# Performance work log

Hardware: AMD Instinct MI355X
Metric: run time of the kernel (lower is better)

The kernel has to match this reference:

```python
import jax, jax.numpy as jnp
import numpy as np

NHEADS = 16
LORA_SCALE = 16.0 / 16.0  # alpha / r


def lora_linear(x, W, b, A, B):
    # base projection + low-rank LoRA path: x@W^T + b + s*(x@A^T)@B^T
    base = jnp.einsum('bse,oe->bso', x, W) + b
    low = jnp.einsum('bse,re->bsr', x, A)  # [B,S,r]
    return base + LORA_SCALE * jnp.einsum('bsr,or->bso', low, B)


def setup_inputs() -> dict:
    key = jax.random.key(0)
    E, R = 1024, 16
    ks = jax.random.split(key, 20)
    d = {'x': jax.random.normal(ks[0], (4, 1024, E), jnp.float32)}
    i = 1
    for p in ('q', 'k', 'v', 'o'):
        d[f'{p}_w'] = jax.random.normal(ks[i], (E, E), jnp.float32) * 0.02; i += 1
        d[f'{p}_b'] = jax.random.normal(ks[i], (E,), jnp.float32) * 0.02; i += 1
        d[f'{p}_la'] = jax.random.normal(ks[i], (R, E), jnp.float32) * 0.02; i += 1
        d[f'{p}_lb'] = jax.random.normal(ks[i], (E, R), jnp.float32) * 0.02; i += 1
    return d


def reference(x, q_w, q_b, q_la, q_lb, k_w, k_b, k_la, k_lb,
              v_w, v_b, v_la, v_lb, o_w, o_b, o_la, o_lb):
    B, S, E = x.shape
    H = NHEADS
    D = E // H
    q = lora_linear(x, q_w, q_b, q_la, q_lb).reshape(B, S, H, D)
    k = lora_linear(x, k_w, k_b, k_la, k_lb).reshape(B, S, H, D)
    v = lora_linear(x, v_w, v_b, v_la, v_lb).reshape(B, S, H, D)
    scores = jnp.einsum('bshd,bthd->bhst', q, k) / jnp.sqrt(jnp.asarray(D, x.dtype))
    attn = jax.nn.softmax(scores, axis=-1)
    ctx = jnp.einsum('bhst,bthd->bshd', attn, v).reshape(B, S, E)
    return lora_linear(ctx, o_w, o_b, o_la, o_lb)
```

## Files before the change

### kernel.cpp

```cpp
#include <hip/hip_runtime.h>
#include <cstdint>


typedef __attribute__((ext_vector_type(8))) short bf16x8;
typedef __attribute__((ext_vector_type(4))) float f32x4;
typedef __attribute__((ext_vector_type(16))) float f32x16;
typedef __attribute__((ext_vector_type(4))) unsigned short u16x4;
typedef __attribute__((ext_vector_type(4))) unsigned int u32x4;

__device__ __forceinline__ short f2bf(float f) {
  unsigned u = __builtin_bit_cast(unsigned, f);
  u += 0x7FFFu + ((u >> 16) & 1u);
  return (short)(u >> 16);
}

typedef __attribute__((address_space(1))) const unsigned int as1_uint;
typedef __attribute__((address_space(3))) unsigned int as3_uint;

__device__ __forceinline__ void gload_lds16(const short* g, const short* l) {
  __builtin_amdgcn_global_load_lds((as1_uint*)g,
      (as3_uint*)(unsigned int)(uintptr_t)l, 16, 0, 0);
}

__device__ __forceinline__ unsigned cvtpk(float lo, float hi) {
  unsigned r;
  asm("v_cvt_pk_bf16_f32 %0, %1, %2" : "=v"(r) : "v"(lo), "v"(hi));
  return r;
}
__device__ __forceinline__ void plswap(unsigned &a, unsigned &b) {
  asm("v_permlane32_swap_b32 %0, %1" : "+v"(a), "+v"(b));
}

__device__ __forceinline__ void build_pfrag(const f32x16 &s, bf16x8 &f0, bf16x8 &f1) {
  unsigned x0 = cvtpk(s[0], s[1]),  x1 = cvtpk(s[2], s[3]);
  unsigned x2 = cvtpk(s[4], s[5]),  x3 = cvtpk(s[6], s[7]);
  plswap(x0, x2); plswap(x1, x3);
  unsigned y0 = cvtpk(s[8], s[9]),  y1 = cvtpk(s[10], s[11]);
  unsigned y2 = cvtpk(s[12], s[13]), y3 = cvtpk(s[14], s[15]);
  plswap(y0, y2); plswap(y1, y3);
  u32x4 a = {x0, x1, x2, x3}, b = {y0, y1, y2, y3};
  f0 = __builtin_bit_cast(bf16x8, a);
  f1 = __builtin_bit_cast(bf16x8, b);
}

__global__ void build_x(const float* __restrict__ x, short* __restrict__ xb) {
  int idx = blockIdx.x * 256 + threadIdx.x;
  f32x4 v = ((const f32x4*)x)[idx];
  u16x4 o;
  o[0] = (unsigned short)f2bf(v[0]);
  o[1] = (unsigned short)f2bf(v[1]);
  o[2] = (unsigned short)f2bf(v[2]);
  o[3] = (unsigned short)f2bf(v[3]);
  ((u16x4*)xb)[idx] = o;
}

__global__ void fold_w(const float* __restrict__ wq, const float* __restrict__ wk,
                       const float* __restrict__ wv, const float* __restrict__ wo,
                       const float* __restrict__ bq, const float* __restrict__ bk,
                       const float* __restrict__ bv, const float* __restrict__ bo,
                       const float* __restrict__ aq, const float* __restrict__ ak,
                       const float* __restrict__ av, const float* __restrict__ ao,
                       short* __restrict__ out) {
  const int p = blockIdx.y;
  const float* W  = (p == 0) ? wq : (p == 1) ? wk : (p == 2) ? wv : wo;
  const float* Bm = (p == 0) ? bq : (p == 1) ? bk : (p == 2) ? bv : bo;
  const float* A  = (p == 0) ? aq : (p == 1) ? ak : (p == 2) ? av : ao;
  const int idx = blockIdx.x * 256 + threadIdx.x;
  const int n = idx >> 8;
  const int e4 = idx & 255;
  f32x4 acc = ((const f32x4*)(W + (size_t)n * 1024))[e4];
  const float* br = Bm + n * 16;
  #pragma unroll
  for (int r = 0; r < 16; ++r) {
    const f32x4 a4 = ((const f32x4*)(A + (size_t)r * 1024))[e4];
    const float b = br[r];
    acc[0] += b * a4[0];
    acc[1] += b * a4[1];
    acc[2] += b * a4[2];
    acc[3] += b * a4[3];
  }
  u16x4 o;
  o[0] = (unsigned short)f2bf(acc[0]);
  o[1] = (unsigned short)f2bf(acc[1]);
  o[2] = (unsigned short)f2bf(acc[2]);
  o[3] = (unsigned short)f2bf(acc[3]);
  *(u16x4*)(out + (size_t)p * 1048576 + (size_t)idx * 4) = o;
}

__device__ __forceinline__ void gemm_core(const short* __restrict__ xrow,
                                          const short* __restrict__ wrow,
                                          short* As, short* Bs,
                                          f32x4 (&acc)[4][4]) {
  const int tid = threadIdx.x;
  const int wv = tid >> 6, lane = tid & 63;
  const int wr = wv >> 1, wc = wv & 1;
  const int lrow = lane & 15, lk = lane >> 4;
  const int srow = lane >> 3, sphys = lane & 7;

  for (int kt = 0; kt < 16; ++kt) {
    #pragma unroll
    for (int i = 0; i < 4; ++i) {
      const int ch = i * 4 + wv;
      const int row = ch * 8 + srow;
      const int sl = sphys ^ (row & 7);
      gload_lds16(xrow + (size_t)row * 1024 + kt * 64 + sl * 8, As + ch * 512);
      gload_lds16(wrow + (size_t)row * 1024 + kt * 64 + sl * 8, Bs + ch * 512);
    }
    __syncthreads();
    #pragma unroll
    for (int kc = 0; kc < 2; ++kc) {
      bf16x8 af[4], bw[4];
      #pragma unroll
      for (int mi = 0; mi < 4; ++mi) {
        const int row = wr * 64 + mi * 16 + lrow;
        const int slot = (kc * 4 + lk) ^ (row & 7);
        af[mi] = *(const bf16x8*)(As + row * 64 + slot * 8);
      }
      #pragma unroll
      for (int nj = 0; nj < 4; ++nj) {
        const int row = wc * 64 + nj * 16 + lrow;
        const int slot = (kc * 4 + lk) ^ (row & 7);
        bw[nj] = *(const bf16x8*)(Bs + row * 64 + slot * 8);
      }
      #pragma unroll
      for (int mi = 0; mi < 4; ++mi)
        #pragma unroll
        for (int nj = 0; nj < 4; ++nj)
          acc[mi][nj] = __builtin_amdgcn_mfma_f32_16x16x32_bf16(af[mi], bw[nj], acc[mi][nj], 0, 0, 0);
    }
    __syncthreads();
  }
}

__global__ __launch_bounds__(256)
void gemm_qkv(const short* __restrict__ xb, const short* __restrict__ wb,
              const float* __restrict__ biasq, const float* __restrict__ biask,
              const float* __restrict__ biasv,
              short* __restrict__ qbuf, short* __restrict__ kbuf, short* __restrict__ vtb) {
  __shared__ short As[128 * 64];
  __shared__ short Bs[128 * 64];
  const int p = blockIdx.z;
  const int brow = blockIdx.y, bcol = blockIdx.x;
  const f32x4 fz = {0.f, 0.f, 0.f, 0.f};
  f32x4 acc[4][4];
  #pragma unroll
  for (int a = 0; a < 4; ++a)
    #pragma unroll
    for (int b = 0; b < 4; ++b) acc[a][b] = fz;

  gemm_core(xb + (size_t)brow * 128 * 1024,
            wb + ((size_t)p * 1024 + (size_t)bcol * 128) * 1024, As, Bs, acc);

  const int tid = threadIdx.x;
  const int wv = tid >> 6, lane = tid & 63;
  const int wr = wv >> 1, wc = wv & 1;
  const int lrow = lane & 15, lk = lane >> 4;
  const float* bias = (p == 0) ? biasq : (p == 1) ? biask : biasv;
  const float oscale = (p == 0) ? 0.18033688f : 1.0f;
  float bcv[4];
  #pragma unroll
  for (int nj = 0; nj < 4; ++nj)
    bcv[nj] = bias[bcol * 128 + wc * 64 + nj * 16 + lrow];

  #pragma unroll
  for (int mi = 0; mi < 4; ++mi) {
    #pragma unroll
    for (int r = 0; r < 4; ++r) {
      const int gr = brow * 128 + wr * 64 + mi * 16 + lk * 4 + r;
      const int bb = gr >> 10, s = gr & 1023;
      #pragma unroll
      for (int nj = 0; nj < 4; ++nj) {
        const int gc = bcol * 128 + wc * 64 + nj * 16 + lrow;
        const float v = (acc[mi][nj][r] + bcv[nj]) * oscale;
        const int h = gc >> 6, d = gc & 63;
        const int bh = bb * 16 + h;
        if (p == 2)
          vtb[((size_t)bh * 64 + d) * 1024 + s] = f2bf(v);
        else
          ((p == 0) ? qbuf : kbuf)[((size_t)bh * 1024 + s) * 64 + d] = f2bf(v);
      }
    }
  }
}

__global__ __launch_bounds__(256)
void attn_kernel(const short* __restrict__ qbuf, const short* __restrict__ kbuf,
                 const short* __restrict__ vtb, short* __restrict__ cb) {
  __shared__ short Ks[2][64 * 64];
  __shared__ short Vs[2][64 * 64];
  const int bh = blockIdx.x, qt = blockIdx.y;
  const int tid = threadIdx.x, w = tid >> 6, lane = tid & 63;
  const int l31 = lane & 31, hi = lane >> 5;
  const int srow = lane >> 3, sphys = lane & 7;
  const short* Qp = qbuf + (size_t)bh * 65536;
  const short* Kp = kbuf + (size_t)bh * 65536;
  const short* Vp = vtb + (size_t)bh * 65536;
  const int q0 = qt * 128 + w * 32;

  bf16x8 bq[4];
  #pragma unroll
  for (int kc = 0; kc < 4; ++kc)
    bq[kc] = *(const bf16x8*)(Qp + (size_t)(q0 + l31) * 64 + kc * 16 + hi * 8);

  const f32x16 fz16 = {0.f,0.f,0.f,0.f,0.f,0.f,0.f,0.f,0.f,0.f,0.f,0.f,0.f,0.f,0.f,0.f};
  float m_run = -1e30f, l_run = 0.f;
  f32x16 acc0 = fz16, acc1 = fz16;

  #define STAGE_KV(buf, tt)                                                  \
    {                                                                        \
      const int t0s = (tt) * 64;                                             \
      _Pragma("unroll")                                                      \
      for (int i = 0; i < 2; ++i) {                                          \
        const int ch = i * 4 + w;                                            \
        const int row = ch * 8 + srow;                                       \
        const int sl = sphys ^ (row & 7);                                    \
        gload_lds16(Kp + (size_t)(t0s + row) * 64 + sl * 8, Ks[buf] + ch * 512); \
        gload_lds16(Vp + (size_t)row * 1024 + t0s + sl * 8, Vs[buf] + ch * 512); \
      }                                                                      \
    }

  STAGE_KV(0, 0);
  __syncthreads();

  int cur = 0;
  for (int tt = 0; tt < 16; ++tt) {
    if (tt < 15) STAGE_KV(cur ^ 1, tt + 1);

    f32x16 s0 = fz16, s1 = fz16;
    #pragma unroll
    for (int kc = 0; kc < 4; ++kc) {
      const int slot = (kc * 2 + hi) ^ (l31 & 7);
      const bf16x8 ak0 = *(const bf16x8*)(Ks[cur] + l31 * 64 + slot * 8);
      const bf16x8 ak1 = *(const bf16x8*)(Ks[cur] + (32 + l31) * 64 + slot * 8);
      s0 = __builtin_amdgcn_mfma_f32_32x32x16_bf16(ak0, bq[kc], s0, 0, 0, 0);
      s1 = __builtin_amdgcn_mfma_f32_32x32x16_bf16(ak1, bq[kc], s1, 0, 0, 0);
    }

    float tm = s0[0];
    #pragma unroll
    for (int r = 1; r < 16; ++r) tm = fmaxf(tm, s0[r]);
    #pragma unroll
    for (int r = 0; r < 16; ++r) tm = fmaxf(tm, s1[r]);
    tm = fmaxf(tm, __shfl_xor(tm, 32, 64));
    const float mn = fmaxf(m_run, tm);
    const float alpha = exp2f(m_run - mn);
    m_run = mn;
    float rs = 0.f;
    #pragma unroll
    for (int r = 0; r < 16; ++r) { const float p = exp2f(s0[r] - mn); s0[r] = p; rs += p; }
    #pragma unroll
    for (int r = 0; r < 16; ++r) { const float p = exp2f(s1[r] - mn); s1[r] = p; rs += p; }
    rs += __shfl_xor(rs, 32, 64);
    l_run = l_run * alpha + rs;
    #pragma unroll
    for (int r = 0; r < 16; ++r) { acc0[r] *= alpha; acc1[r] *= alpha; }

    bf16x8 pf[4];
    build_pfrag(s0, pf[0], pf[1]);
    build_pfrag(s1, pf[2], pf[3]);

    #pragma unroll
    for (int kc4 = 0; kc4 < 4; ++kc4) {
      const int slot = (kc4 * 2 + hi) ^ (l31 & 7);
      const bf16x8 av0 = *(const bf16x8*)(Vs[cur] + l31 * 64 + slot * 8);
      const bf16x8 av1 = *(const bf16x8*)(Vs[cur] + (32 + l31) * 64 + slot * 8);
      acc0 = __builtin_amdgcn_mfma_f32_32x32x16_bf16(av0, pf[kc4], acc0, 0, 0, 0);
      acc1 = __builtin_amdgcn_mfma_f32_32x32x16_bf16(av1, pf[kc4], acc1, 0, 0, 0);
    }

    __syncthreads();
    cur ^= 1;
  }

  const int bb = bh >> 4, h = bh & 15;
  const int s = q0 + l31;
  short* crow = cb + (size_t)(bb * 1024 + s) * 1024 + h * 64;
  const float inv = 1.f / l_run;
  #pragma unroll
  for (int rp = 0; rp < 8; ++rp) {
    const int r = rp * 2;
    const int d = (r & 3) + 8 * (r >> 2) + 4 * hi;
    const unsigned p0 = (unsigned)(unsigned short)f2bf(acc0[r] * inv)
                      | ((unsigned)(unsigned short)f2bf(acc0[r + 1] * inv) << 16);
    const unsigned p1 = (unsigned)(unsigned short)f2bf(acc1[r] * inv)
                      | ((unsigned)(unsigned short)f2bf(acc1[r + 1] * inv) << 16);
    *(unsigned*)(crow + d) = p0;
    *(unsigned*)(crow + 32 + d) = p1;
  }
  #undef STAGE_KV
}

__global__ __launch_bounds__(256)
void gemm_o(const short* __restrict__ cb, const short* __restrict__ wo,
            const float* __restrict__ biaso, float* __restrict__ out) {
  __shared__ short As[128 * 64];
  __shared__ short Bs[128 * 64];
  const int brow = blockIdx.y, bcol = blockIdx.x;
  const f32x4 fz = {0.f, 0.f, 0.f, 0.f};
  f32x4 acc[4][4];
  #pragma unroll
  for (int a = 0; a < 4; ++a)
    #pragma unroll
    for (int b = 0; b < 4; ++b) acc[a][b] = fz;

  gemm_core(cb + (size_t)brow * 128 * 1024, wo + (size_t)bcol * 128 * 1024, As, Bs, acc);

  const int tid = threadIdx.x;
  const int wv = tid >> 6, lane = tid & 63;
  const int wr = wv >> 1, wc = wv & 1;
  const int lrow = lane & 15, lk = lane >> 4;
  float bcv[4];
  #pragma unroll
  for (int nj = 0; nj < 4; ++nj)
    bcv[nj] = biaso[bcol * 128 + wc * 64 + nj * 16 + lrow];

  #pragma unroll
  for (int mi = 0; mi < 4; ++mi) {
    #pragma unroll
    for (int r = 0; r < 4; ++r) {
      const int gr = brow * 128 + wr * 64 + mi * 16 + lk * 4 + r;
      #pragma unroll
      for (int nj = 0; nj < 4; ++nj) {
        const int gc = bcol * 128 + wc * 64 + nj * 16 + lrow;
        out[(size_t)gr * 1024 + gc] = acc[mi][nj][r] + bcv[nj];
      }
    }
  }
}

extern "C" void kernel_launch(void* const* d_in, const int* in_sizes, int n_in,
                              void* d_out, int out_size, void* d_ws, size_t ws_size,
                              hipStream_t stream) {
  (void)in_sizes; (void)n_in; (void)out_size; (void)ws_size;
  const float* x   = (const float*)d_in[0];
  const float* qw  = (const float*)d_in[1];
  const float* qb  = (const float*)d_in[2];
  const float* qla = (const float*)d_in[3];
  const float* qlb = (const float*)d_in[4];
  const float* kw  = (const float*)d_in[5];
  const float* kb  = (const float*)d_in[6];
  const float* kla = (const float*)d_in[7];
  const float* klb = (const float*)d_in[8];
  const float* vw  = (const float*)d_in[9];
  const float* vb  = (const float*)d_in[10];
  const float* vla = (const float*)d_in[11];
  const float* vlb = (const float*)d_in[12];
  const float* ow  = (const float*)d_in[13];
  const float* ob  = (const float*)d_in[14];
  const float* ola = (const float*)d_in[15];
  const float* olb = (const float*)d_in[16];

  short* xb   = (short*)d_ws;
  short* wb   = xb + (size_t)4096 * 1024;
  short* qbuf = wb + (size_t)4 * 1024 * 1024;
  short* kbuf = qbuf + (size_t)4194304;
  short* vtb  = kbuf + (size_t)4194304;

  build_x<<<4096, 256, 0, stream>>>(x, xb);
  fold_w<<<dim3(1024, 4), 256, 0, stream>>>(qw, kw, vw, ow, qlb, klb, vlb, olb,
                                            qla, kla, vla, ola, wb);
  gemm_qkv<<<dim3(8, 32, 3), 256, 0, stream>>>(xb, wb, qb, kb, vb, qbuf, kbuf, vtb);
  attn_kernel<<<dim3(64, 8), 256, 0, stream>>>(qbuf, kbuf, vtb, xb);
  gemm_o<<<dim3(8, 32), 256, 0, stream>>>(xb, wb + (size_t)3 * 1024 * 1024, ob, (float*)d_out);
}
```

Measured before the change: 141.1 us.

## Double-buffer GEMM LDS tiles and remap QKV blocks per XCD for reuse

The shared GEMM core now uses two LDS buffers, so the global-to-LDS loads for the next K tile are issued before the MFMA work on the current tile, and one barrier per iteration is removed. The QKV GEMM launch becomes a flat 1D grid whose block index is remapped so that each XCD handles three adjacent weight column tiles across all row tiles, aiming for better L2 reuse of weights. The cost is doubled LDS per block (64KB), which may reduce occupancy.

```diff
diff --git a/kernel.cpp b/kernel.cpp
--- a/kernel.cpp
+++ b/kernel.cpp
@@ -87,26 +87,33 @@
   *(u16x4*)(out + (size_t)p * 1048576 + (size_t)idx * 4) = o;
 }
 
-__device__ __forceinline__ void gemm_core(const short* __restrict__ xrow,
-                                          const short* __restrict__ wrow,
-                                          short* As, short* Bs,
-                                          f32x4 (&acc)[4][4]) {
+__device__ __forceinline__ void gemm_core_db(const short* __restrict__ xrow,
+                                             const short* __restrict__ wrow,
+                                             short (&As)[2][8192], short (&Bs)[2][8192],
+                                             f32x4 (&acc)[4][4]) {
   const int tid = threadIdx.x;
   const int wv = tid >> 6, lane = tid & 63;
   const int wr = wv >> 1, wc = wv & 1;
   const int lrow = lane & 15, lk = lane >> 4;
   const int srow = lane >> 3, sphys = lane & 7;
 
+#define STAGE_G(buf, kt)                                                       \
+  {                                                                            \
+    _Pragma("unroll")                                                          \
+    for (int i = 0; i < 4; ++i) {                                              \
+      const int ch = i * 4 + wv;                                               \
+      const int row = ch * 8 + srow;                                           \
+      const int sl = sphys ^ (row & 7);                                        \
+      gload_lds16(xrow + (size_t)row * 1024 + (kt) * 64 + sl * 8, As[buf] + ch * 512); \
+      gload_lds16(wrow + (size_t)row * 1024 + (kt) * 64 + sl * 8, Bs[buf] + ch * 512); \
+    }                                                                          \
+  }
+
+  STAGE_G(0, 0);
+  __syncthreads();
+  int cur = 0;
   for (int kt = 0; kt < 16; ++kt) {
-    #pragma unroll
-    for (int i = 0; i < 4; ++i) {
-      const int ch = i * 4 + wv;
-      const int row = ch * 8 + srow;
-      const int sl = sphys ^ (row & 7);
-      gload_lds16(xrow + (size_t)row * 1024 + kt * 64 + sl * 8, As + ch * 512);
-      gload_lds16(wrow + (size_t)row * 1024 + kt * 64 + sl * 8, Bs + ch * 512);
-    }
-    __syncthreads();
+    if (kt < 15) STAGE_G(cur ^ 1, kt + 1);
     #pragma unroll
     for (int kc = 0; kc < 2; ++kc) {
       bf16x8 af[4], bw[4];
@@ -114,13 +121,13 @@
       for (int mi = 0; mi < 4; ++mi) {
         const int row = wr * 64 + mi * 16 + lrow;
         const int slot = (kc * 4 + lk) ^ (row & 7);
-        af[mi] = *(const bf16x8*)(As + row * 64 + slot * 8);
+        af[mi] = *(const bf16x8*)(As[cur] + row * 64 + slot * 8);
       }
       #pragma unroll
       for (int nj = 0; nj < 4; ++nj) {
         const int row = wc * 64 + nj * 16 + lrow;
         const int slot = (kc * 4 + lk) ^ (row & 7);
-        bw[nj] = *(const bf16x8*)(Bs + row * 64 + slot * 8);
+        bw[nj] = *(const bf16x8*)(Bs[cur] + row * 64 + slot * 8);
       }
       #pragma unroll
       for (int mi = 0; mi < 4; ++mi)
@@ -129,7 +136,9 @@
           acc[mi][nj] = __builtin_amdgcn_mfma_f32_16x16x32_bf16(af[mi], bw[nj], acc[mi][nj], 0, 0, 0);
     }
     __syncthreads();
-  }
+    cur ^= 1;
+  }
+#undef STAGE_G
 }
 
 __global__ __launch_bounds__(256)
@@ -137,10 +146,14 @@
               const float* __restrict__ biasq, const float* __restrict__ biask,
               const float* __restrict__ biasv,
               short* __restrict__ qbuf, short* __restrict__ kbuf, short* __restrict__ vtb) {
-  __shared__ short As[128 * 64];
-  __shared__ short Bs[128 * 64];
-  const int p = blockIdx.z;
-  const int brow = blockIdx.y, bcol = blockIdx.x;
+  __shared__ short As[2][8192];
+  __shared__ short Bs[2][8192];
+  const int wg = blockIdx.x;
+  const int xcd = wg & 7, ix = wg >> 3;
+  const int bcol = xcd * 3 + ix % 3;
+  const int brow = ix / 3;
+  const int p = bcol >> 3;
+
   const f32x4 fz = {0.f, 0.f, 0.f, 0.f};
   f32x4 acc[4][4];
   #pragma unroll
@@ -148,8 +161,8 @@
     #pragma unroll
     for (int b = 0; b < 4; ++b) acc[a][b] = fz;
 
-  gemm_core(xb + (size_t)brow * 128 * 1024,
-            wb + ((size_t)p * 1024 + (size_t)bcol * 128) * 1024, As, Bs, acc);
+  gemm_core_db(xb + (size_t)brow * 128 * 1024,
+               wb + (size_t)bcol * 128 * 1024, As, Bs, acc);
 
   const int tid = threadIdx.x;
   const int wv = tid >> 6, lane = tid & 63;
@@ -157,10 +170,11 @@
   const int lrow = lane & 15, lk = lane >> 4;
   const float* bias = (p == 0) ? biasq : (p == 1) ? biask : biasv;
   const float oscale = (p == 0) ? 0.18033688f : 1.0f;
+  const int c0 = (bcol & 7) * 128;
   float bcv[4];
   #pragma unroll
   for (int nj = 0; nj < 4; ++nj)
-    bcv[nj] = bias[bcol * 128 + wc * 64 + nj * 16 + lrow];
+    bcv[nj] = bias[c0 + wc * 64 + nj * 16 + lrow];
 
   #pragma unroll
   for (int mi = 0; mi < 4; ++mi) {
@@ -170,7 +184,7 @@
       const int bb = gr >> 10, s = gr & 1023;
       #pragma unroll
       for (int nj = 0; nj < 4; ++nj) {
-        const int gc = bcol * 128 + wc * 64 + nj * 16 + lrow;
+        const int gc = c0 + wc * 64 + nj * 16 + lrow;
         const float v = (acc[mi][nj][r] + bcv[nj]) * oscale;
         const int h = gc >> 6, d = gc & 63;
         const int bh = bb * 16 + h;
@@ -293,8 +307,8 @@
 __global__ __launch_bounds__(256)
 void gemm_o(const short* __restrict__ cb, const short* __restrict__ wo,
             const float* __restrict__ biaso, float* __restrict__ out) {
-  __shared__ short As[128 * 64];
-  __shared__ short Bs[128 * 64];
+  __shared__ short As[2][8192];
+  __shared__ short Bs[2][8192];
   const int brow = blockIdx.y, bcol = blockIdx.x;
   const f32x4 fz = {0.f, 0.f, 0.f, 0.f};
   f32x4 acc[4][4];
@@ -303,7 +317,8 @@
     #pragma unroll
     for (int b = 0; b < 4; ++b) acc[a][b] = fz;
 
-  gemm_core(cb + (size_t)brow * 128 * 1024, wo + (size_t)bcol * 128 * 1024, As, Bs, acc);
+  gemm_core_db(cb + (size_t)brow * 128 * 1024, wo + (size_t)bcol * 128 * 1024,
+               As, Bs, acc);
 
   const int tid = threadIdx.x;
   const int wv = tid >> 6, lane = tid & 63;
@@ -359,7 +374,7 @@
   build_x<<<4096, 256, 0, stream>>>(x, xb);
   fold_w<<<dim3(1024, 4), 256, 0, stream>>>(qw, kw, vw, ow, qlb, klb, vlb, olb,
                                             qla, kla, vla, ola, wb);
-  gemm_qkv<<<dim3(8, 32, 3), 256, 0, stream>>>(xb, wb, qb, kb, vb, qbuf, kbuf, vtb);
+  gemm_qkv<<<768, 256, 0, stream>>>(xb, wb, qb, kb, vb, qbuf, kbuf, vtb);
   attn_kernel<<<dim3(64, 8), 256, 0, stream>>>(qbuf, kbuf, vtb, xb);
   gemm_o<<<dim3(8, 32), 256, 0, stream>>>(xb, wb + (size_t)3 * 1024 * 1024, ob, (float*)d_out);
 }
```

Result: faster. 137.3 us (-2.7%).
